# Kernel optimization log

Hardware: AMD Instinct MI355X
Metric: run time of the kernel (lower is better)

Reference implementation:

```python
import jax, jax.numpy as jnp
import numpy as np

P = 16
BN_EPS = 1e-5


def _to_patches(x, c, d):
    # [b, c*P, d*P] -> [b, c*d, P, P]
    b = x.shape[0]
    x = x.reshape(b, c, P, d, P).transpose(0, 1, 3, 2, 4)
    return x.reshape(b, c * d, P, P)


def _dwconv_block(x, dwk, g, bb, m, v, pwk):
    # depthwise 3x3 stride-2 conv (groups=C, no bias) + BN(eval) + GELU + 1x1 pointwise
    C = x.shape[1]
    y = jax.lax.conv_general_dilated(
        x, dwk[:, None, :, :], window_strides=(2, 2), padding=((1, 1), (1, 1)),
        feature_group_count=C, dimension_numbers=('NCHW', 'OIHW', 'NCHW'))
    y = g[None, :, None, None] * (y - m[None, :, None, None]) / jnp.sqrt(v + BN_EPS)[None, :, None, None] + bb[None, :, None, None]
    y = jax.nn.gelu(y, approximate=False)  # torch nn.GELU default = erf
    return jnp.einsum('bchw,oc->bohw', y, pwk)


def _forward(query, key, value, dw_k, bn_g, bn_b, bn_m, bn_v, pw_k, position, c1_w, c1_b, lin_w, lin_b):
    b, units, d_model = query.shape
    c = units // P
    d = d_model // P
    hp = P // 2  # spatial after stride-2 conv
    dk = hp * hp  # d_k = 64

    q = _to_patches(query, c, d)
    k = _to_patches(key, c, d)
    v = _to_patches(value, c, d)

    q = _dwconv_block(q, dw_k[0], bn_g[0], bn_b[0], bn_m[0], bn_v[0], pw_k[0])
    k = _dwconv_block(k, dw_k[1], bn_g[1], bn_b[1], bn_m[1], bn_v[1], pw_k[1])
    v = _dwconv_block(v, dw_k[2], bn_g[2], bn_b[2], bn_m[2], bn_v[2], pw_k[2])

    # [b, c*d, hp, hp] -> [b, c, d, hp*hp]
    q = q.reshape(b, c, d, dk)
    k = k.reshape(b, c, d, dk)
    v = v.reshape(b, c, d, dk)

    scores = jnp.einsum('bcdk,bcek->bcde', q, k) / jnp.sqrt(jnp.asarray(dk, q.dtype))
    scores = scores + position[None]  # learned additive position bias [c,d,d]
    p_attn = jax.nn.softmax(scores, axis=-1)
    x = jnp.einsum('bcde,bcek->bcdk', p_attn, v)  # [b, c, d, dk]

    # 'b c d (p1 p2) -> b (c p1) (d p2)', p1 = P//2
    x = x.reshape(b, c, d, hp, hp).transpose(0, 1, 3, 2, 4).reshape(b, c * hp, d * hp)

    # Conv1d(units//2 -> units, kernel 1) then Linear(d_model//2 -> d_model)
    x = jnp.einsum('bcl,oc->bol', x, c1_w) + c1_b[None, :, None]
    x = jnp.einsum('bcl,ol->bco', x, lin_w) + lin_b[None, None, :]
    return x


def setup_inputs() -> dict:
    key = jax.random.key(0)
    ks = jax.random.split(key, 8)
    b, units, d_model = 64, 32, 4096
    C = (units // P) * (d_model // P)  # 512
    inp = {
        'query': jax.random.normal(ks[0], (b, units, d_model), jnp.float32),
        'key': jax.random.normal(ks[1], (b, units, d_model), jnp.float32),
        'value': jax.random.normal(ks[2], (b, units, d_model), jnp.float32),
        'dw_k': jax.random.normal(ks[3], (3, C, 3, 3), jnp.float32) * 0.1,
        'bn_g': jnp.ones((3, C), jnp.float32),
        'bn_b': jnp.zeros((3, C), jnp.float32),
        'bn_m': jnp.zeros((3, C), jnp.float32),
        'bn_v': jnp.ones((3, C), jnp.float32),
        'pw_k': jax.random.normal(ks[4], (3, C, C), jnp.float32) * 0.02,
        'position': jax.random.normal(ks[5], (units // P, d_model // P, d_model // P), jnp.float32),
        'c1_w': jax.random.normal(ks[6], (units, units // 2), jnp.float32) * 0.1,
        'c1_b': jnp.zeros((units,), jnp.float32),
        'lin_w': jax.random.normal(ks[7], (d_model, d_model // 2), jnp.float32) * 0.02,
        'lin_b': jnp.zeros((d_model,), jnp.float32),
    }
    return inp


def reference(query, key, value, dw_k, bn_g, bn_b, bn_m, bn_v, pw_k, position, c1_w, c1_b, lin_w, lin_b):
    return _forward(query, key, value, dw_k, bn_g, bn_b, bn_m, bn_v, pw_k, position, c1_w, c1_b, lin_w, lin_b)
```

## Files before the change

### kernel.cpp

```cpp
#include <hip/hip_runtime.h>


typedef short s16x8 __attribute__((ext_vector_type(8)));
typedef float f32x4 __attribute__((ext_vector_type(4)));
typedef const __attribute__((address_space(1))) void* gas_t;
typedef __attribute__((address_space(3))) void* las_t;

__device__ __forceinline__ unsigned short f2bf(float x) {
  unsigned u = __float_as_uint(x);
  unsigned r = u + 0x7fffu + ((u >> 16) & 1u);
  return (unsigned short)(r >> 16);
}
__device__ __forceinline__ float bf2f(unsigned short h) {
  return __uint_as_float((unsigned)h << 16);
}

__global__ __launch_bounds__(256) void stageA_kernel(
    const float* __restrict__ xq, const float* __restrict__ xk,
    const float* __restrict__ xv, const float* __restrict__ dwk,
    const float* __restrict__ bng, const float* __restrict__ bnb,
    const float* __restrict__ bnm, const float* __restrict__ bnv,
    unsigned short* __restrict__ tTp)
{
  const int i  = blockIdx.y;
  const float* x = (i == 0) ? xq : (i == 1) ? xk : xv;
  const float* dwk_i = dwk + (size_t)i * 4608;
  const int co = i * 512;
  unsigned short* out = tTp + (size_t)i * 4194304;

  const int dd = threadIdx.x;
  const int oh = blockIdx.x & 7;
  const int cc = (blockIdx.x >> 3) & 1;
  const int b  = blockIdx.x >> 4;
  const int ch = cc * 256 + dd;

  float r[3][16];
#pragma unroll
  for (int kh = 0; kh < 3; ++kh) {
    int ih = 2 * oh - 1 + kh;
    if (ih >= 0 && ih <= 15) {
      const float* p = x + (size_t)(b * 32 + cc * 16 + ih) * 4096 + dd * 16;
#pragma unroll
      for (int jq = 0; jq < 4; ++jq)
        *(float4*)&r[kh][jq * 4] = *(const float4*)(p + jq * 4);
    } else {
#pragma unroll
      for (int j = 0; j < 16; ++j) r[kh][j] = 0.f;
    }
  }
  float w9[9];
#pragma unroll
  for (int j = 0; j < 9; ++j) w9[j] = dwk_i[ch * 9 + j];
  const float scale = bng[co + ch] / sqrtf(bnv[co + ch] + 1e-5f);
  const float shift = bnb[co + ch] - bnm[co + ch] * scale;

#pragma unroll
  for (int ow = 0; ow < 8; ++ow) {
    float acc = 0.f;
#pragma unroll
    for (int kh = 0; kh < 3; ++kh)
#pragma unroll
      for (int kw = 0; kw < 3; ++kw) {
        int iw = 2 * ow - 1 + kw;
        if (iw >= 0 && iw <= 15) acc = fmaf(r[kh][iw], w9[kh * 3 + kw], acc);
      }
    float y = acc * scale + shift;
    y = 0.5f * y * (1.f + erff(y * 0.70710678118654752f));
    unsigned short hi = f2bf(y);
    unsigned short lo = f2bf(y - bf2f(hi));
    size_t rowb = (size_t)(b * 64 + oh * 8 + ow) * 1024;
    out[rowb + ch] = hi;
    out[rowb + 512 + ch] = lo;
  }
}

__global__ __launch_bounds__(256) void split_kernel(
    const float* __restrict__ src, unsigned short* __restrict__ dst,
    int kshift, int total4)
{
  int i = blockIdx.x * 256 + threadIdx.x;
  if (i >= total4) return;
  size_t i4 = (size_t)i * 4;
  int K = 1 << kshift;
  int r = (int)(i4 >> kshift);
  int c = (int)(i4 & (size_t)(K - 1));
  float4 xv = *(const float4*)(src + i4);
  unsigned short h0 = f2bf(xv.x), h1 = f2bf(xv.y), h2 = f2bf(xv.z), h3 = f2bf(xv.w);
  unsigned short l0 = f2bf(xv.x - bf2f(h0)), l1 = f2bf(xv.y - bf2f(h1));
  unsigned short l2 = f2bf(xv.z - bf2f(h2)), l3 = f2bf(xv.w - bf2f(h3));
  unsigned short* dr = dst + (size_t)r * (K * 2) + c;
  uint2 hp, lp;
  hp.x = (unsigned)h0 | ((unsigned)h1 << 16);
  hp.y = (unsigned)h2 | ((unsigned)h3 << 16);
  lp.x = (unsigned)l0 | ((unsigned)l1 << 16);
  lp.y = (unsigned)l2 | ((unsigned)l3 << 16);
  *(uint2*)dr = hp;
  *(uint2*)(dr + K) = lp;
}

__global__ __launch_bounds__(256) void split_rs_kernel(
    const float* __restrict__ src, unsigned short* __restrict__ dst,
    float* __restrict__ rs, int total4)
{
  int i = blockIdx.x * 256 + threadIdx.x;
  if (i >= total4) return;
  size_t i4 = (size_t)i * 4;
  int r = (int)(i4 >> 11);
  int c = (int)(i4 & 2047);
  float4 xv = *(const float4*)(src + i4);
  unsigned short h0 = f2bf(xv.x), h1 = f2bf(xv.y), h2 = f2bf(xv.z), h3 = f2bf(xv.w);
  unsigned short l0 = f2bf(xv.x - bf2f(h0)), l1 = f2bf(xv.y - bf2f(h1));
  unsigned short l2 = f2bf(xv.z - bf2f(h2)), l3 = f2bf(xv.w - bf2f(h3));
  unsigned short* dr = dst + (size_t)r * 4096 + c;
  uint2 hp, lp;
  hp.x = (unsigned)h0 | ((unsigned)h1 << 16);
  hp.y = (unsigned)h2 | ((unsigned)h3 << 16);
  lp.x = (unsigned)l0 | ((unsigned)l1 << 16);
  lp.y = (unsigned)l2 | ((unsigned)l3 << 16);
  *(uint2*)dr = hp;
  *(uint2*)(dr + 2048) = lp;
  float s = xv.x + xv.y + xv.z + xv.w;
#pragma unroll
  for (int off = 1; off < 64; off <<= 1) s += __shfl_xor(s, off, 64);
  if ((threadIdx.x & 63) == 0) atomicAdd(&rs[r], s);
}

__global__ __launch_bounds__(256) void gemm_split_kernel(
    const unsigned short* __restrict__ Aall, const unsigned short* __restrict__ Ball,
    unsigned short* __restrict__ Call, int M, int N, int K)
{
  __shared__ unsigned short sA[4096];
  __shared__ unsigned short sB[8192];
  const int t = threadIdx.x;
  const int z = blockIdx.z;
  const unsigned short* A = Aall + (size_t)z * 524288;
  const unsigned short* B = Ball + (size_t)z * 4194304;
  unsigned short* Cq = Call + (size_t)z * 4194304;
  const int m0 = blockIdx.y * 64, n0 = blockIdx.x * 128;
  const int Kp = 3 * K, twoK = 2 * K, Km = K - 1;
  const int lane = t & 63;
  const int wv = t >> 6;
  const int colbase = wv * 32;
  const int h = lane & 15, g = lane >> 4;

  f32x4 acc[4][2];
#pragma unroll
  for (int mf = 0; mf < 4; ++mf)
#pragma unroll
    for (int nf = 0; nf < 2; ++nf)
      acc[mf][nf] = (f32x4){0.f, 0.f, 0.f, 0.f};

  int srow[4], sblk[4];
#pragma unroll
  for (int it = 0; it < 4; ++it) {
    int s = it * 256 + t;
    srow[it] = s >> 3;
    sblk[it] = (s & 7) ^ (srow[it] & 7);
  }
  const int ldsw = (t & 192) << 4;

  for (int k0 = 0; k0 < Kp; k0 += 64) {
    __syncthreads();
#pragma unroll
    for (int it = 0; it < 2; ++it) {
      int kp = k0 + sblk[it] * 8;
      int ac = (kp < twoK) ? (kp & Km) : (kp - K);
      const unsigned short* ga = A + (size_t)(m0 + srow[it]) * twoK + ac;
      __builtin_amdgcn_global_load_lds((gas_t)(const void*)ga,
          (las_t)(void*)((char*)sA + (it * 4096 + ldsw)), 16, 0, 0);
    }
#pragma unroll
    for (int it = 0; it < 4; ++it) {
      int kp = k0 + sblk[it] * 8;
      int bc = (kp < twoK) ? kp : (kp - twoK);
      const unsigned short* gb = B + (size_t)(n0 + srow[it]) * twoK + bc;
      __builtin_amdgcn_global_load_lds((gas_t)(const void*)gb,
          (las_t)(void*)((char*)sB + (it * 4096 + ldsw)), 16, 0, 0);
    }
    __syncthreads();

#pragma unroll
    for (int kk = 0; kk < 2; ++kk) {
      s16x8 af[4], bfr[2];
#pragma unroll
      for (int mf = 0; mf < 4; ++mf) {
        int arow = mf * 16 + h;
        int aoff = arow * 128 + (((kk * 4 + g) ^ (h & 7)) << 4);
        af[mf] = *(const s16x8*)((const char*)sA + aoff);
      }
#pragma unroll
      for (int nf = 0; nf < 2; ++nf) {
        int brow = colbase + nf * 16 + h;
        int boff = brow * 128 + (((kk * 4 + g) ^ (h & 7)) << 4);
        bfr[nf] = *(const s16x8*)((const char*)sB + boff);
      }
#pragma unroll
      for (int mf = 0; mf < 4; ++mf)
#pragma unroll
        for (int nf = 0; nf < 2; ++nf)
          acc[mf][nf] = __builtin_amdgcn_mfma_f32_16x16x32_bf16(
              af[mf], bfr[nf], acc[mf][nf], 0, 0, 0);
    }
  }

  if (z < 2) {
#pragma unroll
    for (int mf = 0; mf < 4; ++mf) {
      int mbase = m0 + mf * 16 + g * 4;
#pragma unroll
      for (int nf = 0; nf < 2; ++nf) {
        int n = n0 + colbase + nf * 16 + h;
        int bb = n >> 6, d = n & 63;
#pragma unroll
        for (int qq = 0; qq < 4; ++qq) {
          int m = mbase + qq;
          int cc = m >> 8;
          size_t rowb = ((size_t)(bb * 2 + cc) * 256 + (m & 255)) * 128;
          float vvv = acc[mf][nf][qq];
          unsigned short hi = f2bf(vvv);
          unsigned short lo = f2bf(vvv - bf2f(hi));
          Cq[rowb + d] = hi;
          Cq[rowb + 64 + d] = lo;
        }
      }
    }
  } else {
#pragma unroll
    for (int mf = 0; mf < 4; ++mf) {
      int mbase = m0 + mf * 16 + g * 4;
      int cc = mbase >> 8;
      int mc = mbase & 255;
#pragma unroll
      for (int nf = 0; nf < 2; ++nf) {
        int n = n0 + colbase + nf * 16 + h;
        int bb = n >> 6, d = n & 63;
        size_t rowb = ((size_t)(bb * 2 + cc) * 64 + d) * 512;
        ushort4 hv, lv;
        float v0 = acc[mf][nf][0], v1 = acc[mf][nf][1];
        float v2 = acc[mf][nf][2], v3 = acc[mf][nf][3];
        hv.x = f2bf(v0); hv.y = f2bf(v1); hv.z = f2bf(v2); hv.w = f2bf(v3);
        lv.x = f2bf(v0 - bf2f(hv.x)); lv.y = f2bf(v1 - bf2f(hv.y));
        lv.z = f2bf(v2 - bf2f(hv.z)); lv.w = f2bf(v3 - bf2f(hv.w));
        *(ushort4*)&Cq[rowb + mc] = hv;
        *(ushort4*)&Cq[rowb + 256 + mc] = lv;
      }
    }
  }
}

__global__ __launch_bounds__(256, 2) void gemm_final_kernel(
    const unsigned short* __restrict__ A, const unsigned short* __restrict__ B,
    float* __restrict__ C, int M, int N, int K)
{
  __shared__ unsigned short lds[36864];
  const int t = threadIdx.x;

  const int flat = blockIdx.y * 32 + blockIdx.x;
  const int xcd = flat & 7;
  const int ii = flat >> 3;
  const int n0 = (xcd * 4 + (ii & 3)) * 128;
  const int m0 = (ii >> 2) * 64;

  const int twoK = 2 * K, Km = K - 1;
  const int nt = (3 * K) >> 6;

  const int lane = t & 63;
  const int wv = t >> 6;
  const int colbase = wv * 32;
  const int h = lane & 15, g = lane >> 4;

  f32x4 acc[4][2];
#pragma unroll
  for (int mf = 0; mf < 4; ++mf)
#pragma unroll
    for (int nf = 0; nf < 2; ++nf)
      acc[mf][nf] = (f32x4){0.f, 0.f, 0.f, 0.f};

  int arow[2], ablk[2], brow[4], bblk[4];
#pragma unroll
  for (int it = 0; it < 2; ++it) {
    int s = it * 256 + t;
    arow[it] = s >> 3;
    ablk[it] = (s & 7) ^ (arow[it] & 7);
  }
#pragma unroll
  for (int it = 0; it < 4; ++it) {
    int s = it * 256 + t;
    brow[it] = s >> 3;
    bblk[it] = (s & 7) ^ (brow[it] & 7);
  }

  auto issueA = [&](int buf, int tt, int it) {
    int kp = tt * 64 + ablk[it] * 8;
    int ac = (kp < twoK) ? (kp & Km) : (kp - K);
    __builtin_amdgcn_global_load_lds(
        (gas_t)(const void*)(A + (size_t)(m0 + arow[it]) * twoK + ac),
        (las_t)(void*)((char*)lds + (buf * 24576 + it * 4096 + t * 16)), 16, 0, 0);
  };
  auto issueB = [&](int buf, int tt, int it) {
    int kp = tt * 64 + bblk[it] * 8;
    int bc = (kp < twoK) ? kp : (kp - twoK);
    __builtin_amdgcn_global_load_lds(
        (gas_t)(const void*)(B + (size_t)(n0 + brow[it]) * twoK + bc),
        (las_t)(void*)((char*)lds + (buf * 24576 + 8192 + it * 4096 + t * 16)), 16, 0, 0);
  };

  int colx[2];
  colx[0] = ((g) ^ (h & 7)) << 4;
  colx[1] = ((4 + g) ^ (h & 7)) << 4;

  auto rdA = [&](int buf, int kk, int mf) -> s16x8 {
    return *(const s16x8*)((const char*)lds +
        (buf * 24576 + (mf * 16 + h) * 128 + colx[kk]));
  };
  auto rdB = [&](int buf, int kk, int nf) -> s16x8 {
    return *(const s16x8*)((const char*)lds +
        (buf * 24576 + 8192 + (colbase + nf * 16 + h) * 128 + colx[kk]));
  };

#define MFMA8(A0, A1, A2, A3, B0, B1) \
  acc[0][0] = __builtin_amdgcn_mfma_f32_16x16x32_bf16(A0, B0, acc[0][0], 0, 0, 0); \
  acc[1][0] = __builtin_amdgcn_mfma_f32_16x16x32_bf16(A1, B0, acc[1][0], 0, 0, 0); \
  acc[2][0] = __builtin_amdgcn_mfma_f32_16x16x32_bf16(A2, B0, acc[2][0], 0, 0, 0); \
  acc[3][0] = __builtin_amdgcn_mfma_f32_16x16x32_bf16(A3, B0, acc[3][0], 0, 0, 0); \
  acc[0][1] = __builtin_amdgcn_mfma_f32_16x16x32_bf16(A0, B1, acc[0][1], 0, 0, 0); \
  acc[1][1] = __builtin_amdgcn_mfma_f32_16x16x32_bf16(A1, B1, acc[1][1], 0, 0, 0); \
  acc[2][1] = __builtin_amdgcn_mfma_f32_16x16x32_bf16(A2, B1, acc[2][1], 0, 0, 0); \
  acc[3][1] = __builtin_amdgcn_mfma_f32_16x16x32_bf16(A3, B1, acc[3][1], 0, 0, 0);

#pragma unroll
  for (int it = 0; it < 2; ++it) issueA(0, 0, it);
#pragma unroll
  for (int it = 0; it < 4; ++it) issueB(0, 0, it);
#pragma unroll
  for (int it = 0; it < 2; ++it) issueA(1, 1, it);
#pragma unroll
  for (int it = 0; it < 4; ++it) issueB(1, 1, it);
  asm volatile("s_waitcnt vmcnt(6)" ::: "memory");
  __builtin_amdgcn_sched_barrier(0);
  __builtin_amdgcn_s_barrier();
  __builtin_amdgcn_sched_barrier(0);

  int bR = 0;
  for (int tt = 0; tt <= nt - 3; ++tt) {
    const int bn2 = (bR >= 1) ? bR - 1 : 2;
    s16x8 a0 = rdA(bR, 0, 0), a1 = rdA(bR, 0, 1), a2 = rdA(bR, 0, 2), a3 = rdA(bR, 0, 3);
    s16x8 b0 = rdB(bR, 0, 0), b1 = rdB(bR, 0, 1);
    issueA(bn2, tt + 2, 0); issueA(bn2, tt + 2, 1); issueB(bn2, tt + 2, 0);
    __builtin_amdgcn_s_barrier();
    __builtin_amdgcn_s_setprio(1);
    MFMA8(a0, a1, a2, a3, b0, b1)
    __builtin_amdgcn_s_setprio(0);
    __builtin_amdgcn_s_barrier();
    a0 = rdA(bR, 1, 0); a1 = rdA(bR, 1, 1); a2 = rdA(bR, 1, 2); a3 = rdA(bR, 1, 3);
    b0 = rdB(bR, 1, 0); b1 = rdB(bR, 1, 1);
    issueB(bn2, tt + 2, 1); issueB(bn2, tt + 2, 2); issueB(bn2, tt + 2, 3);
    __builtin_amdgcn_s_barrier();
    __builtin_amdgcn_s_setprio(1);
    MFMA8(a0, a1, a2, a3, b0, b1)
    __builtin_amdgcn_s_setprio(0);
    asm volatile("s_waitcnt vmcnt(6)" ::: "memory");
    __builtin_amdgcn_sched_barrier(0);
    __builtin_amdgcn_s_barrier();
    __builtin_amdgcn_sched_barrier(0);
    bR = (bR == 2) ? 0 : bR + 1;
  }

  auto compute_tile = [&](int buf) {
#pragma unroll
    for (int kk = 0; kk < 2; ++kk) {
      s16x8 ta0 = rdA(buf, kk, 0), ta1 = rdA(buf, kk, 1);
      s16x8 ta2 = rdA(buf, kk, 2), ta3 = rdA(buf, kk, 3);
      s16x8 tb0 = rdB(buf, kk, 0), tb1 = rdB(buf, kk, 1);
      MFMA8(ta0, ta1, ta2, ta3, tb0, tb1)
    }
  };
  compute_tile(bR);
  __syncthreads();
  compute_tile((bR == 2) ? 0 : bR + 1);
#undef MFMA8

#pragma unroll
  for (int mf = 0; mf < 4; ++mf) {
    int mbase = m0 + mf * 16 + g * 4;
#pragma unroll
    for (int nf = 0; nf < 2; ++nf) {
      int n = n0 + colbase + nf * 16 + h;
#pragma unroll
      for (int qq = 0; qq < 4; ++qq)
        C[(size_t)(mbase + qq) * N + n] = acc[mf][nf][qq];
    }
  }
}

__global__ __launch_bounds__(256) void attn_mfma_kernel(
    const unsigned short* __restrict__ qp, const unsigned short* __restrict__ kp,
    const unsigned short* __restrict__ vtp, const float* __restrict__ pos,
    unsigned short* __restrict__ Xp)
{
  __shared__ char smem[59904];
  unsigned short* qs = (unsigned short*)smem;
  unsigned short* kv = (unsigned short*)(smem + 8704);
  float* sc = (float*)(smem + 26112);
  unsigned short* ps = (unsigned short*)(smem + 26112);

  const int t = threadIdx.x;
  const int rt = blockIdx.x, cc = blockIdx.y, b = blockIdx.z;
  const int i0 = rt * 32;
  const size_t qkbase = (size_t)(b * 2 + cc) * 256;
  const size_t vbase  = (size_t)(b * 2 + cc) * 64;

  const int lane = t & 63, wvv = t >> 6;
  const int h = lane & 15, g = lane >> 4;

#pragma unroll
  for (int rep = 0; rep < 2; ++rep) {
    int s = t + rep * 256;
    int row = s >> 4;
    int blk = s & 15;
    int4 val = *(const int4*)(qp + (qkbase + i0 + row) * 128 + blk * 8);
    *(int4*)((char*)qs + row * 272 + blk * 16) = val;
  }

  for (int c = 0; c < 4; ++c) {
    __syncthreads();
#pragma unroll
    for (int p2 = 0; p2 < 4; ++p2) {
      int s = t + p2 * 256;
      int row = s >> 4;
      int blk = s & 15;
      int4 val = *(const int4*)(kp + (qkbase + c * 64 + row) * 128 + blk * 8);
      *(int4*)((char*)kv + row * 272 + blk * 16) = val;
    }
    __syncthreads();
    f32x4 acc2[2];
    acc2[0] = (f32x4){0.f, 0.f, 0.f, 0.f};
    acc2[1] = (f32x4){0.f, 0.f, 0.f, 0.f};
#pragma unroll
    for (int kk = 0; kk < 6; ++kk) {
      int abase = (kk < 2) ? kk * 32 : (kk < 4) ? 64 + (kk - 2) * 32 : (kk - 4) * 32;
      int bbase = (kk < 2) ? kk * 32 : (kk < 4) ? (kk - 2) * 32 : 64 + (kk - 4) * 32;
      s16x8 bfrag = *(const s16x8*)((char*)kv + (wvv * 16 + h) * 272 + (bbase + g * 8) * 2);
#pragma unroll
      for (int mf = 0; mf < 2; ++mf) {
        s16x8 afrag = *(const s16x8*)((char*)qs + (mf * 16 + h) * 272 + (abase + g * 8) * 2);
        acc2[mf] = __builtin_amdgcn_mfma_f32_16x16x32_bf16(afrag, bfrag, acc2[mf], 0, 0, 0);
      }
    }
#pragma unroll
    for (int mf = 0; mf < 2; ++mf)
#pragma unroll
      for (int qq = 0; qq < 4; ++qq) {
        int row = mf * 16 + g * 4 + qq;
        int j = c * 64 + wvv * 16 + h;
        sc[row * 264 + j] = acc2[mf][qq] * 0.125f +
            pos[((size_t)cc * 256 + i0 + row) * 256 + j];
      }
  }
  __syncthreads();

  {
    const int r = t >> 3, j8 = t & 7;
    float e[32];
    float mx = -3.4e38f;
#pragma unroll
    for (int jj = 0; jj < 32; ++jj) {
      e[jj] = sc[r * 264 + j8 + 8 * jj];
      mx = fmaxf(mx, e[jj]);
    }
#pragma unroll
    for (int mset = 1; mset < 8; mset <<= 1) mx = fmaxf(mx, __shfl_xor(mx, mset, 64));
    float sum = 0.f;
#pragma unroll
    for (int jj = 0; jj < 32; ++jj) {
      e[jj] = expf(e[jj] - mx);
      sum += e[jj];
    }
#pragma unroll
    for (int mset = 1; mset < 8; mset <<= 1) sum += __shfl_xor(sum, mset, 64);
    float inv = 1.f / sum;
    __syncthreads();
#pragma unroll
    for (int jj = 0; jj < 32; ++jj) {
      float pv = e[jj] * inv;
      unsigned short hi = f2bf(pv);
      unsigned short lo = f2bf(pv - bf2f(hi));
      int j = j8 + 8 * jj;
      ps[r * 528 + j] = hi;
      ps[r * 528 + 264 + j] = lo;
    }
  }

  f32x4 oacc[2];
  oacc[0] = (f32x4){0.f, 0.f, 0.f, 0.f};
  oacc[1] = (f32x4){0.f, 0.f, 0.f, 0.f};
  for (int c = 0; c < 4; ++c) {
    __syncthreads();
#pragma unroll
    for (int p2 = 0; p2 < 4; ++p2) {
      int s = t + p2 * 256, row = s >> 4, blk = s & 15;
      int col = (blk < 8) ? (c * 64 + blk * 8) : (256 + c * 64 + (blk - 8) * 8);
      int4 val = *(const int4*)(vtp + (vbase + row) * 512 + col);
      *(int4*)((char*)kv + row * 272 + blk * 16) = val;
    }
    __syncthreads();
#pragma unroll
    for (int kk = 0; kk < 6; ++kk) {
      int abase = (kk < 2) ? (c * 64 + kk * 32)
                : (kk < 4) ? (264 + c * 64 + (kk - 2) * 32)
                           : (c * 64 + (kk - 4) * 32);
      int bbase = (kk < 2) ? kk * 32 : (kk < 4) ? (kk - 2) * 32 : 64 + (kk - 4) * 32;
      s16x8 bfrag = *(const s16x8*)((char*)kv + (wvv * 16 + h) * 272 + (bbase + g * 8) * 2);
#pragma unroll
      for (int mf = 0; mf < 2; ++mf) {
        s16x8 afrag = *(const s16x8*)((char*)ps + (mf * 16 + h) * 1056 + (abase + g * 8) * 2);
        oacc[mf] = __builtin_amdgcn_mfma_f32_16x16x32_bf16(afrag, bfrag, oacc[mf], 0, 0, 0);
      }
    }
  }
  {
    int Xrow = b * 16 + cc * 8 + wvv * 2 + (h >> 3);
    int c7 = h & 7;
#pragma unroll
    for (int mf = 0; mf < 2; ++mf)
#pragma unroll
      for (int qq = 0; qq < 4; ++qq) {
        int dd = i0 + mf * 16 + g * 4 + qq;
        float vvv = oacc[mf][qq];
        unsigned short hi = f2bf(vvv);
        unsigned short lo = f2bf(vvv - bf2f(hi));
        size_t base = (size_t)Xrow * 4096 + dd * 8 + c7;
        Xp[base] = hi;
        Xp[base + 2048] = lo;
      }
  }
}

__global__ __launch_bounds__(256) void epilogue_kernel(
    const float* __restrict__ G, const float* __restrict__ rs,
    const float* __restrict__ c1w, const float* __restrict__ c1b,
    const float* __restrict__ linb, float* __restrict__ out)
{
  __shared__ float W[512];
  __shared__ float Bp[32];
  const int t = threadIdx.x;
  const int ntile = blockIdx.x;
  const int b = blockIdx.y;
  W[t] = c1w[t];
  W[t + 256] = c1w[t + 256];
  if (t < 32) Bp[t] = c1b[t];
  __syncthreads();
  const int n = ntile * 256 + t;
  float gv[16];
#pragma unroll
  for (int ch = 0; ch < 16; ++ch)
    gv[ch] = G[(size_t)(b * 16 + ch) * 4096 + n];
  const float rsn = rs[n];
  const float lbn = linb[n];
#pragma unroll
  for (int o = 0; o < 32; ++o) {
    float s = lbn + Bp[o] * rsn;
#pragma unroll
    for (int ch = 0; ch < 16; ++ch) s = fmaf(W[o * 16 + ch], gv[ch], s);
    out[(size_t)(b * 32 + o) * 4096 + n] = s;
  }
}

extern "C" void kernel_launch(void* const* d_in, const int* in_sizes, int n_in,
                              void* d_out, int out_size, void* d_ws, size_t ws_size,
                              hipStream_t stream) {
  const float* q    = (const float*)d_in[0];
  const float* k    = (const float*)d_in[1];
  const float* v    = (const float*)d_in[2];
  const float* dwk  = (const float*)d_in[3];
  const float* bng  = (const float*)d_in[4];
  const float* bnb  = (const float*)d_in[5];
  const float* bnm  = (const float*)d_in[6];
  const float* bnv  = (const float*)d_in[7];
  const float* pwk  = (const float*)d_in[8];
  const float* pos  = (const float*)d_in[9];
  const float* c1w  = (const float*)d_in[10];
  const float* c1b  = (const float*)d_in[11];
  const float* linw = (const float*)d_in[12];
  const float* linb = (const float*)d_in[13];
  float* out = (float*)d_out;

  if (ws_size < 50331648u) return;

  char* ws = (char*)d_ws;
  unsigned short* qp   = (unsigned short*)(ws + 0);
  unsigned short* kpp  = (unsigned short*)(ws + 8388608);
  unsigned short* vtp  = (unsigned short*)(ws + 16777216);
  unsigned short* tTp  = (unsigned short*)(ws + 25165824);
  unsigned short* pwkp = (unsigned short*)d_out;
  unsigned short* Xp   = (unsigned short*)(ws + 25165824);
  float*          rs   = (float*)(ws + 0);
  unsigned short* lwp  = (unsigned short*)d_out;
  float*          G    = (float*)(ws + 33554432);

  split_kernel<<<768, 256, 0, stream>>>(pwk, pwkp, 9, 196608);

  stageA_kernel<<<dim3(1024, 3), 256, 0, stream>>>(
      q, k, v, dwk, bng, bnb, bnm, bnv, tTp);

  gemm_split_kernel<<<dim3(32, 8, 3), 256, 0, stream>>>(
      pwkp, tTp, qp, 512, 4096, 512);

  attn_mfma_kernel<<<dim3(8, 2, 64), 256, 0, stream>>>(qp, kpp, vtp, pos, Xp);

  hipMemsetAsync(rs, 0, 16384, stream);
  split_rs_kernel<<<8192, 256, 0, stream>>>(linw, lwp, rs, 2097152);

  gemm_final_kernel<<<dim3(32, 16), 256, 0, stream>>>(Xp, lwp, G, 1024, 4096, 2048);

  epilogue_kernel<<<dim3(16, 64), 256, 0, stream>>>(G, rs, c1w, c1b, linb, out);
}
```

Before: 187.8 us.

## Triple-buffer pointwise GEMM with async LDS prefetch and XCD-aware block mapping

Rewrites the split-bf16 pointwise-conv GEMM as a three-stage LDS ring. Global-to-LDS loads for tile t+2 are issued while MFMAs run on tile t, with waitcnt and barriers interleaved and setprio raised around the MFMA groups. It also remaps the flat block index so neighbouring N tiles land on the same XCD for L2 reuse, and hardcodes K and occupancy 2. The cost is more LDS per block (72KB) and tightly hand-scheduled synchronization that is fragile to get right.

```diff
diff --git a/kernel.cpp b/kernel.cpp
--- a/kernel.cpp
+++ b/kernel.cpp
@@ -125,19 +125,27 @@
   if ((threadIdx.x & 63) == 0) atomicAdd(&rs[r], s);
 }
 
-__global__ __launch_bounds__(256) void gemm_split_kernel(
+__global__ __launch_bounds__(256, 2) void gemm_pw_pipe_kernel(
     const unsigned short* __restrict__ Aall, const unsigned short* __restrict__ Ball,
-    unsigned short* __restrict__ Call, int M, int N, int K)
+    unsigned short* __restrict__ Call)
 {
-  __shared__ unsigned short sA[4096];
-  __shared__ unsigned short sB[8192];
+  __shared__ unsigned short lds[36864];
   const int t = threadIdx.x;
-  const int z = blockIdx.z;
+
+  const int flat = (blockIdx.z * 8 + blockIdx.y) * 32 + blockIdx.x;
+  const int xcd = flat & 7;
+  const int ii = flat >> 3;
+  const int n0 = (xcd * 4 + (ii & 3)) * 128;
+  const int rem = ii >> 2;
+  const int m0 = (rem & 7) * 64;
+  const int z = rem >> 3;
+
   const unsigned short* A = Aall + (size_t)z * 524288;
   const unsigned short* B = Ball + (size_t)z * 4194304;
   unsigned short* Cq = Call + (size_t)z * 4194304;
-  const int m0 = blockIdx.y * 64, n0 = blockIdx.x * 128;
-  const int Kp = 3 * K, twoK = 2 * K, Km = K - 1;
+
+  const int K = 512, twoK = 1024, Km = 511, nt = 24;
+
   const int lane = t & 63;
   const int wv = t >> 6;
   const int colbase = wv * 32;
@@ -150,58 +158,109 @@
     for (int nf = 0; nf < 2; ++nf)
       acc[mf][nf] = (f32x4){0.f, 0.f, 0.f, 0.f};
 
-  int srow[4], sblk[4];
+  int arow[2], ablk[2], brow[4], bblk[4];
+#pragma unroll
+  for (int it = 0; it < 2; ++it) {
+    int s = it * 256 + t;
+    arow[it] = s >> 3;
+    ablk[it] = (s & 7) ^ (arow[it] & 7);
+  }
 #pragma unroll
   for (int it = 0; it < 4; ++it) {
     int s = it * 256 + t;
-    srow[it] = s >> 3;
-    sblk[it] = (s & 7) ^ (srow[it] & 7);
-  }
-  const int ldsw = (t & 192) << 4;
-
-  for (int k0 = 0; k0 < Kp; k0 += 64) {
-    __syncthreads();
-#pragma unroll
-    for (int it = 0; it < 2; ++it) {
-      int kp = k0 + sblk[it] * 8;
-      int ac = (kp < twoK) ? (kp & Km) : (kp - K);
-      const unsigned short* ga = A + (size_t)(m0 + srow[it]) * twoK + ac;
-      __builtin_amdgcn_global_load_lds((gas_t)(const void*)ga,
-          (las_t)(void*)((char*)sA + (it * 4096 + ldsw)), 16, 0, 0);
-    }
-#pragma unroll
-    for (int it = 0; it < 4; ++it) {
-      int kp = k0 + sblk[it] * 8;
-      int bc = (kp < twoK) ? kp : (kp - twoK);
-      const unsigned short* gb = B + (size_t)(n0 + srow[it]) * twoK + bc;
-      __builtin_amdgcn_global_load_lds((gas_t)(const void*)gb,
-          (las_t)(void*)((char*)sB + (it * 4096 + ldsw)), 16, 0, 0);
-    }
-    __syncthreads();
-
+    brow[it] = s >> 3;
+    bblk[it] = (s & 7) ^ (brow[it] & 7);
+  }
+
+  auto issueA = [&](int buf, int tt, int it) {
+    int kp = tt * 64 + ablk[it] * 8;
+    int ac = (kp < twoK) ? (kp & Km) : (kp - K);
+    __builtin_amdgcn_global_load_lds(
+        (gas_t)(const void*)(A + (size_t)(m0 + arow[it]) * twoK + ac),
+        (las_t)(void*)((char*)lds + (buf * 24576 + it * 4096 + t * 16)), 16, 0, 0);
+  };
+  auto issueB = [&](int buf, int tt, int it) {
+    int kp = tt * 64 + bblk[it] * 8;
+    int bc = (kp < twoK) ? kp : (kp - twoK);
+    __builtin_amdgcn_global_load_lds(
+        (gas_t)(const void*)(B + (size_t)(n0 + brow[it]) * twoK + bc),
+        (las_t)(void*)((char*)lds + (buf * 24576 + 8192 + it * 4096 + t * 16)), 16, 0, 0);
+  };
+
+  int colx[2];
+  colx[0] = ((g) ^ (h & 7)) << 4;
+  colx[1] = ((4 + g) ^ (h & 7)) << 4;
+
+  auto rdA = [&](int buf, int kk, int mf) -> s16x8 {
+    return *(const s16x8*)((const char*)lds +
+        (buf * 24576 + (mf * 16 + h) * 128 + colx[kk]));
+  };
+  auto rdB = [&](int buf, int kk, int nf) -> s16x8 {
+    return *(const s16x8*)((const char*)lds +
+        (buf * 24576 + 8192 + (colbase + nf * 16 + h) * 128 + colx[kk]));
+  };
+
+#define MFMA8(A0, A1, A2, A3, B0, B1) \
+  acc[0][0] = __builtin_amdgcn_mfma_f32_16x16x32_bf16(A0, B0, acc[0][0], 0, 0, 0); \
+  acc[1][0] = __builtin_amdgcn_mfma_f32_16x16x32_bf16(A1, B0, acc[1][0], 0, 0, 0); \
+  acc[2][0] = __builtin_amdgcn_mfma_f32_16x16x32_bf16(A2, B0, acc[2][0], 0, 0, 0); \
+  acc[3][0] = __builtin_amdgcn_mfma_f32_16x16x32_bf16(A3, B0, acc[3][0], 0, 0, 0); \
+  acc[0][1] = __builtin_amdgcn_mfma_f32_16x16x32_bf16(A0, B1, acc[0][1], 0, 0, 0); \
+  acc[1][1] = __builtin_amdgcn_mfma_f32_16x16x32_bf16(A1, B1, acc[1][1], 0, 0, 0); \
+  acc[2][1] = __builtin_amdgcn_mfma_f32_16x16x32_bf16(A2, B1, acc[2][1], 0, 0, 0); \
+  acc[3][1] = __builtin_amdgcn_mfma_f32_16x16x32_bf16(A3, B1, acc[3][1], 0, 0, 0);
+
+#pragma unroll
+  for (int it = 0; it < 2; ++it) issueA(0, 0, it);
+#pragma unroll
+  for (int it = 0; it < 4; ++it) issueB(0, 0, it);
+#pragma unroll
+  for (int it = 0; it < 2; ++it) issueA(1, 1, it);
+#pragma unroll
+  for (int it = 0; it < 4; ++it) issueB(1, 1, it);
+  asm volatile("s_waitcnt vmcnt(6)" ::: "memory");
+  __builtin_amdgcn_sched_barrier(0);
+  __builtin_amdgcn_s_barrier();
+  __builtin_amdgcn_sched_barrier(0);
+
+  int bR = 0;
+  for (int tt = 0; tt <= nt - 3; ++tt) {
+    const int bn2 = (bR >= 1) ? bR - 1 : 2;
+    s16x8 a0 = rdA(bR, 0, 0), a1 = rdA(bR, 0, 1), a2 = rdA(bR, 0, 2), a3 = rdA(bR, 0, 3);
+    s16x8 b0 = rdB(bR, 0, 0), b1 = rdB(bR, 0, 1);
+    issueA(bn2, tt + 2, 0); issueA(bn2, tt + 2, 1); issueB(bn2, tt + 2, 0);
+    __builtin_amdgcn_s_barrier();
+    __builtin_amdgcn_s_setprio(1);
+    MFMA8(a0, a1, a2, a3, b0, b1)
+    __builtin_amdgcn_s_setprio(0);
+    __builtin_amdgcn_s_barrier();
+    a0 = rdA(bR, 1, 0); a1 = rdA(bR, 1, 1); a2 = rdA(bR, 1, 2); a3 = rdA(bR, 1, 3);
+    b0 = rdB(bR, 1, 0); b1 = rdB(bR, 1, 1);
+    issueB(bn2, tt + 2, 1); issueB(bn2, tt + 2, 2); issueB(bn2, tt + 2, 3);
+    __builtin_amdgcn_s_barrier();
+    __builtin_amdgcn_s_setprio(1);
+    MFMA8(a0, a1, a2, a3, b0, b1)
+    __builtin_amdgcn_s_setprio(0);
+    asm volatile("s_waitcnt vmcnt(6)" ::: "memory");
+    __builtin_amdgcn_sched_barrier(0);
+    __builtin_amdgcn_s_barrier();
+    __builtin_amdgcn_sched_barrier(0);
+    bR = (bR == 2) ? 0 : bR + 1;
+  }
+
+  auto compute_tile = [&](int buf) {
 #pragma unroll
     for (int kk = 0; kk < 2; ++kk) {
-      s16x8 af[4], bfr[2];
-#pragma unroll
-      for (int mf = 0; mf < 4; ++mf) {
-        int arow = mf * 16 + h;
-        int aoff = arow * 128 + (((kk * 4 + g) ^ (h & 7)) << 4);
-        af[mf] = *(const s16x8*)((const char*)sA + aoff);
-      }
-#pragma unroll
-      for (int nf = 0; nf < 2; ++nf) {
-        int brow = colbase + nf * 16 + h;
-        int boff = brow * 128 + (((kk * 4 + g) ^ (h & 7)) << 4);
-        bfr[nf] = *(const s16x8*)((const char*)sB + boff);
-      }
-#pragma unroll
-      for (int mf = 0; mf < 4; ++mf)
-#pragma unroll
-        for (int nf = 0; nf < 2; ++nf)
-          acc[mf][nf] = __builtin_amdgcn_mfma_f32_16x16x32_bf16(
-              af[mf], bfr[nf], acc[mf][nf], 0, 0, 0);
-    }
-  }
+      s16x8 ta0 = rdA(buf, kk, 0), ta1 = rdA(buf, kk, 1);
+      s16x8 ta2 = rdA(buf, kk, 2), ta3 = rdA(buf, kk, 3);
+      s16x8 tb0 = rdB(buf, kk, 0), tb1 = rdB(buf, kk, 1);
+      MFMA8(ta0, ta1, ta2, ta3, tb0, tb1)
+    }
+  };
+  compute_tile(bR);
+  __syncthreads();
+  compute_tile((bR == 2) ? 0 : bR + 1);
+#undef MFMA8
 
   if (z < 2) {
 #pragma unroll
@@ -603,8 +662,7 @@
   stageA_kernel<<<dim3(1024, 3), 256, 0, stream>>>(
       q, k, v, dwk, bng, bnb, bnm, bnv, tTp);
 
-  gemm_split_kernel<<<dim3(32, 8, 3), 256, 0, stream>>>(
-      pwkp, tTp, qp, 512, 4096, 512);
+  gemm_pw_pipe_kernel<<<dim3(32, 8, 3), 256, 0, stream>>>(pwkp, tTp, qp);
 
   attn_mfma_kernel<<<dim3(8, 2, 64), 256, 0, stream>>>(qp, kpp, vtp, pos, Xp);
 
```

Measured after the change: 191.1 us. Within noise of the previous version (+1.7%).

## Enlarge final GEMM tile to 256x128 with 512 threads and split-K by two

Applied to the files above, without the earlier changes.

The final bf16 split-precision GEMM moves from 64x128 tiles with 256 threads to 256x128 tiles with 512 threads (8 waves, each 64x64). The K loop is split in two halves across blocks, and each half writes its own partial output buffer. The epilogue sums the two partials when it reads G. The aim is more reuse of each LDS load per MFMA and fewer redundant B reads, at the cost of doubled LDS use (96KB per block), lower occupancy, an extra partial buffer write and read, and workspace remapping.

```diff
diff --git a/kernel.cpp b/kernel.cpp
--- a/kernel.cpp
+++ b/kernel.cpp
@@ -248,46 +248,48 @@
   }
 }
 
-__global__ __launch_bounds__(256, 2) void gemm_final_kernel(
+__global__ __launch_bounds__(512, 2) void gemm_final_kernel(
     const unsigned short* __restrict__ A, const unsigned short* __restrict__ B,
-    float* __restrict__ C, int M, int N, int K)
+    float* __restrict__ C)
 {
-  __shared__ unsigned short lds[36864];
+  __shared__ unsigned short lds[73728];
   const int t = threadIdx.x;
 
   const int flat = blockIdx.y * 32 + blockIdx.x;
   const int xcd = flat & 7;
   const int ii = flat >> 3;
   const int n0 = (xcd * 4 + (ii & 3)) * 128;
-  const int m0 = (ii >> 2) * 64;
-
-  const int twoK = 2 * K, Km = K - 1;
-  const int nt = (3 * K) >> 6;
+  const int rem = ii >> 2;
+  const int m0 = (rem & 3) * 256;
+  const int ks = rem >> 2;
+  const int base = ks * 48;
+
+  const int K = 2048, twoK = 4096, Km = 2047;
 
   const int lane = t & 63;
   const int wv = t >> 6;
-  const int colbase = wv * 32;
+  const int wm = wv & 3, wn = wv >> 2;
   const int h = lane & 15, g = lane >> 4;
 
-  f32x4 acc[4][2];
+  f32x4 acc[4][4];
 #pragma unroll
   for (int mf = 0; mf < 4; ++mf)
 #pragma unroll
-    for (int nf = 0; nf < 2; ++nf)
+    for (int nf = 0; nf < 4; ++nf)
       acc[mf][nf] = (f32x4){0.f, 0.f, 0.f, 0.f};
 
-  int arow[2], ablk[2], brow[4], bblk[4];
+  int arow[4], ablk[4], brow[2], bblk[2];
+#pragma unroll
+  for (int it = 0; it < 4; ++it) {
+    int s = it * 512 + t;
+    arow[it] = s >> 3;
+    ablk[it] = (t & 7) ^ (arow[it] & 7);
+  }
 #pragma unroll
   for (int it = 0; it < 2; ++it) {
-    int s = it * 256 + t;
-    arow[it] = s >> 3;
-    ablk[it] = (s & 7) ^ (arow[it] & 7);
-  }
-#pragma unroll
-  for (int it = 0; it < 4; ++it) {
-    int s = it * 256 + t;
+    int s = it * 512 + t;
     brow[it] = s >> 3;
-    bblk[it] = (s & 7) ^ (brow[it] & 7);
+    bblk[it] = (t & 7) ^ (brow[it] & 7);
   }
 
   auto issueA = [&](int buf, int tt, int it) {
@@ -295,69 +297,83 @@
     int ac = (kp < twoK) ? (kp & Km) : (kp - K);
     __builtin_amdgcn_global_load_lds(
         (gas_t)(const void*)(A + (size_t)(m0 + arow[it]) * twoK + ac),
-        (las_t)(void*)((char*)lds + (buf * 24576 + it * 4096 + t * 16)), 16, 0, 0);
+        (las_t)(void*)((char*)lds + (buf * 49152 + it * 8192 + t * 16)), 16, 0, 0);
   };
   auto issueB = [&](int buf, int tt, int it) {
     int kp = tt * 64 + bblk[it] * 8;
     int bc = (kp < twoK) ? kp : (kp - twoK);
     __builtin_amdgcn_global_load_lds(
         (gas_t)(const void*)(B + (size_t)(n0 + brow[it]) * twoK + bc),
-        (las_t)(void*)((char*)lds + (buf * 24576 + 8192 + it * 4096 + t * 16)), 16, 0, 0);
+        (las_t)(void*)((char*)lds + (buf * 49152 + 32768 + it * 8192 + t * 16)), 16, 0, 0);
   };
 
+  const int aoffb = (wm * 64 + h) * 128;
+  const int boffb = 32768 + (wn * 64 + h) * 128;
   int colx[2];
   colx[0] = ((g) ^ (h & 7)) << 4;
   colx[1] = ((4 + g) ^ (h & 7)) << 4;
 
   auto rdA = [&](int buf, int kk, int mf) -> s16x8 {
-    return *(const s16x8*)((const char*)lds +
-        (buf * 24576 + (mf * 16 + h) * 128 + colx[kk]));
+    return *(const s16x8*)((const char*)lds + (buf * 49152 + aoffb + mf * 2048 + colx[kk]));
   };
   auto rdB = [&](int buf, int kk, int nf) -> s16x8 {
-    return *(const s16x8*)((const char*)lds +
-        (buf * 24576 + 8192 + (colbase + nf * 16 + h) * 128 + colx[kk]));
+    return *(const s16x8*)((const char*)lds + (buf * 49152 + boffb + nf * 2048 + colx[kk]));
   };
 
-#define MFMA8(A0, A1, A2, A3, B0, B1) \
-  acc[0][0] = __builtin_amdgcn_mfma_f32_16x16x32_bf16(A0, B0, acc[0][0], 0, 0, 0); \
-  acc[1][0] = __builtin_amdgcn_mfma_f32_16x16x32_bf16(A1, B0, acc[1][0], 0, 0, 0); \
-  acc[2][0] = __builtin_amdgcn_mfma_f32_16x16x32_bf16(A2, B0, acc[2][0], 0, 0, 0); \
-  acc[3][0] = __builtin_amdgcn_mfma_f32_16x16x32_bf16(A3, B0, acc[3][0], 0, 0, 0); \
-  acc[0][1] = __builtin_amdgcn_mfma_f32_16x16x32_bf16(A0, B1, acc[0][1], 0, 0, 0); \
-  acc[1][1] = __builtin_amdgcn_mfma_f32_16x16x32_bf16(A1, B1, acc[1][1], 0, 0, 0); \
-  acc[2][1] = __builtin_amdgcn_mfma_f32_16x16x32_bf16(A2, B1, acc[2][1], 0, 0, 0); \
-  acc[3][1] = __builtin_amdgcn_mfma_f32_16x16x32_bf16(A3, B1, acc[3][1], 0, 0, 0);
-
-#pragma unroll
-  for (int it = 0; it < 2; ++it) issueA(0, 0, it);
-#pragma unroll
-  for (int it = 0; it < 4; ++it) issueB(0, 0, it);
-#pragma unroll
-  for (int it = 0; it < 2; ++it) issueA(1, 1, it);
-#pragma unroll
-  for (int it = 0; it < 4; ++it) issueB(1, 1, it);
+#define MFMA_ROW2(A0, A1, A2, A3, BB, NF) \
+  acc[0][NF] = __builtin_amdgcn_mfma_f32_16x16x32_bf16(A0, BB, acc[0][NF], 0, 0, 0); \
+  acc[1][NF] = __builtin_amdgcn_mfma_f32_16x16x32_bf16(A1, BB, acc[1][NF], 0, 0, 0); \
+  acc[2][NF] = __builtin_amdgcn_mfma_f32_16x16x32_bf16(A2, BB, acc[2][NF], 0, 0, 0); \
+  acc[3][NF] = __builtin_amdgcn_mfma_f32_16x16x32_bf16(A3, BB, acc[3][NF], 0, 0, 0);
+
+#pragma unroll
+  for (int it = 0; it < 4; ++it) issueA(0, base, it);
+#pragma unroll
+  for (int it = 0; it < 2; ++it) issueB(0, base, it);
+#pragma unroll
+  for (int it = 0; it < 4; ++it) issueA(1, base + 1, it);
+#pragma unroll
+  for (int it = 0; it < 2; ++it) issueB(1, base + 1, it);
   asm volatile("s_waitcnt vmcnt(6)" ::: "memory");
   __builtin_amdgcn_sched_barrier(0);
   __builtin_amdgcn_s_barrier();
   __builtin_amdgcn_sched_barrier(0);
 
   int bR = 0;
-  for (int tt = 0; tt <= nt - 3; ++tt) {
+  for (int tt = base; tt <= base + 45; ++tt) {
     const int bn2 = (bR >= 1) ? bR - 1 : 2;
     s16x8 a0 = rdA(bR, 0, 0), a1 = rdA(bR, 0, 1), a2 = rdA(bR, 0, 2), a3 = rdA(bR, 0, 3);
     s16x8 b0 = rdB(bR, 0, 0), b1 = rdB(bR, 0, 1);
-    issueA(bn2, tt + 2, 0); issueA(bn2, tt + 2, 1); issueB(bn2, tt + 2, 0);
+    issueA(bn2, tt + 2, 0); issueA(bn2, tt + 2, 1);
     __builtin_amdgcn_s_barrier();
     __builtin_amdgcn_s_setprio(1);
-    MFMA8(a0, a1, a2, a3, b0, b1)
+    MFMA_ROW2(a0, a1, a2, a3, b0, 0)
+    MFMA_ROW2(a0, a1, a2, a3, b1, 1)
+    __builtin_amdgcn_s_setprio(0);
+    __builtin_amdgcn_s_barrier();
+    s16x8 b2 = rdB(bR, 0, 2), b3 = rdB(bR, 0, 3);
+    issueA(bn2, tt + 2, 2); issueA(bn2, tt + 2, 3);
+    __builtin_amdgcn_s_barrier();
+    __builtin_amdgcn_s_setprio(1);
+    MFMA_ROW2(a0, a1, a2, a3, b2, 2)
+    MFMA_ROW2(a0, a1, a2, a3, b3, 3)
     __builtin_amdgcn_s_setprio(0);
     __builtin_amdgcn_s_barrier();
     a0 = rdA(bR, 1, 0); a1 = rdA(bR, 1, 1); a2 = rdA(bR, 1, 2); a3 = rdA(bR, 1, 3);
     b0 = rdB(bR, 1, 0); b1 = rdB(bR, 1, 1);
-    issueB(bn2, tt + 2, 1); issueB(bn2, tt + 2, 2); issueB(bn2, tt + 2, 3);
+    issueB(bn2, tt + 2, 0);
     __builtin_amdgcn_s_barrier();
     __builtin_amdgcn_s_setprio(1);
-    MFMA8(a0, a1, a2, a3, b0, b1)
+    MFMA_ROW2(a0, a1, a2, a3, b0, 0)
+    MFMA_ROW2(a0, a1, a2, a3, b1, 1)
+    __builtin_amdgcn_s_setprio(0);
+    __builtin_amdgcn_s_barrier();
+    b2 = rdB(bR, 1, 2); b3 = rdB(bR, 1, 3);
+    issueB(bn2, tt + 2, 1);
+    __builtin_amdgcn_s_barrier();
+    __builtin_amdgcn_s_setprio(1);
+    MFMA_ROW2(a0, a1, a2, a3, b2, 2)
+    MFMA_ROW2(a0, a1, a2, a3, b3, 3)
     __builtin_amdgcn_s_setprio(0);
     asm volatile("s_waitcnt vmcnt(6)" ::: "memory");
     __builtin_amdgcn_sched_barrier(0);
@@ -372,23 +388,28 @@
       s16x8 ta0 = rdA(buf, kk, 0), ta1 = rdA(buf, kk, 1);
       s16x8 ta2 = rdA(buf, kk, 2), ta3 = rdA(buf, kk, 3);
       s16x8 tb0 = rdB(buf, kk, 0), tb1 = rdB(buf, kk, 1);
-      MFMA8(ta0, ta1, ta2, ta3, tb0, tb1)
+      s16x8 tb2 = rdB(buf, kk, 2), tb3 = rdB(buf, kk, 3);
+      MFMA_ROW2(ta0, ta1, ta2, ta3, tb0, 0)
+      MFMA_ROW2(ta0, ta1, ta2, ta3, tb1, 1)
+      MFMA_ROW2(ta0, ta1, ta2, ta3, tb2, 2)
+      MFMA_ROW2(ta0, ta1, ta2, ta3, tb3, 3)
     }
   };
   compute_tile(bR);
   __syncthreads();
   compute_tile((bR == 2) ? 0 : bR + 1);
-#undef MFMA8
-
+#undef MFMA_ROW2
+
+  float* Cks = C + (size_t)ks * 4194304;
 #pragma unroll
   for (int mf = 0; mf < 4; ++mf) {
-    int mbase = m0 + mf * 16 + g * 4;
-#pragma unroll
-    for (int nf = 0; nf < 2; ++nf) {
-      int n = n0 + colbase + nf * 16 + h;
+    int mbase = m0 + wm * 64 + mf * 16 + g * 4;
+#pragma unroll
+    for (int nf = 0; nf < 4; ++nf) {
+      int n = n0 + wn * 64 + nf * 16 + h;
 #pragma unroll
       for (int qq = 0; qq < 4; ++qq)
-        C[(size_t)(mbase + qq) * N + n] = acc[mf][nf][qq];
+        Cks[(size_t)(mbase + qq) * 4096 + n] = acc[mf][nf][qq];
     }
   }
 }
@@ -553,8 +574,10 @@
   const int n = ntile * 256 + t;
   float gv[16];
 #pragma unroll
-  for (int ch = 0; ch < 16; ++ch)
-    gv[ch] = G[(size_t)(b * 16 + ch) * 4096 + n];
+  for (int ch = 0; ch < 16; ++ch) {
+    size_t off = (size_t)(b * 16 + ch) * 4096 + n;
+    gv[ch] = G[off] + G[4194304 + off];
+  }
   const float rsn = rs[n];
   const float lbn = linb[n];
 #pragma unroll
@@ -593,10 +616,10 @@
   unsigned short* vtp  = (unsigned short*)(ws + 16777216);
   unsigned short* tTp  = (unsigned short*)(ws + 25165824);
   unsigned short* pwkp = (unsigned short*)d_out;
-  unsigned short* Xp   = (unsigned short*)(ws + 25165824);
+  unsigned short* Xp   = (unsigned short*)(ws + 41943040);
   float*          rs   = (float*)(ws + 0);
   unsigned short* lwp  = (unsigned short*)d_out;
-  float*          G    = (float*)(ws + 33554432);
+  float*          G    = (float*)(ws + 8388608);
 
   split_kernel<<<768, 256, 0, stream>>>(pwk, pwkp, 9, 196608);
 
@@ -611,7 +634,7 @@
   hipMemsetAsync(rs, 0, 16384, stream);
   split_rs_kernel<<<8192, 256, 0, stream>>>(linw, lwp, rs, 2097152);
 
-  gemm_final_kernel<<<dim3(32, 16), 256, 0, stream>>>(Xp, lwp, G, 1024, 4096, 2048);
+  gemm_final_kernel<<<dim3(32, 8), 512, 0, stream>>>(Xp, lwp, G);
 
   epilogue_kernel<<<dim3(16, 64), 256, 0, stream>>>(G, rs, c1w, c1b, linb, out);
 }
```

After: 182.6 us. 1.03x faster.
